# Kernel optimization log

Hardware: AMD Instinct MI355X
Metric: run time of the kernel (lower is better)

The kernel has to match this reference:

```python
import jax, jax.numpy as jnp
import numpy as np

DIM = 1024
HEADS = 16
HEAD_DIM = DIM // HEADS
SEQ = 2048
BATCH = 2


def setup_inputs() -> dict:
    key = jax.random.key(0)
    ks = jax.random.split(key, 9)
    s = 1.0 / np.sqrt(DIM)
    mk = lambda k: jax.random.uniform(k, (DIM, DIM), jnp.float32, -s, s)
    mb = lambda k: jax.random.uniform(k, (DIM,), jnp.float32, -s, s)
    return {
        "x": jax.random.normal(ks[0], (BATCH, SEQ, DIM), jnp.float32),
        "wq": mk(ks[1]), "bq": mb(ks[2]),
        "wk": mk(ks[3]), "bk": mb(ks[4]),
        "wv": mk(ks[5]), "bv": mb(ks[6]),
        "wo": mk(ks[7]), "bo": mb(ks[8]),
    }


def reference(x, wq, bq, wk, bk, wv, bv, wo, bo):
    b, s, d = x.shape
    inv_sqrt_hd = 1.0 / np.sqrt(HEAD_DIM)
    # torch Linear: y = x @ W.T + b
    q = (x @ wq.T + bq).reshape(b, s, HEADS, HEAD_DIM)
    k = (x @ wk.T + bk).reshape(b, s, HEADS, HEAD_DIM)
    v = (x @ wv.T + bv).reshape(b, s, HEADS, HEAD_DIM)
    # scores [b, h, s, s]; NOTE: original forward never applies the causal mask buffer
    scores = jnp.einsum("bqhd,bkhd->bhqk", q, k) * inv_sqrt_hd
    a = jax.nn.softmax(scores, axis=-1)
    o = jnp.einsum("bhqk,bkhd->bqhd", a, v).reshape(b, s, d)
    o = o @ wo.T + bo
    return (o, a.mean(axis=1))
```

## Files before the change

### kernel.cpp

```cpp
#include <hip/hip_runtime.h>
#include <stdint.h>

#define DIMD 1024
#define HEADS 16
#define HD 64
#define SEQ 2048
#define BATCH 2
#define MTOT (BATCH*SEQ)

typedef __attribute__((ext_vector_type(4))) float f32x4;
typedef __attribute__((ext_vector_type(8))) short bf16x8;
typedef __attribute__((ext_vector_type(8))) unsigned short ushort8;
typedef __attribute__((ext_vector_type(4))) unsigned short usx4;

#define GL_LDS16(gp, lp) __builtin_amdgcn_global_load_lds( \
    (const __attribute__((address_space(1))) unsigned int*)(gp), \
    (__attribute__((address_space(3))) unsigned int*)(lp), 16, 0, 0)

__device__ __forceinline__ unsigned short f2bf(float f) {
    unsigned int u = __builtin_bit_cast(unsigned int, f);
    u = (u + 0x7FFFu + ((u >> 16) & 1u)) >> 16;
    return (unsigned short)u;
}
__device__ __forceinline__ float bf2f(unsigned short s) {
    unsigned int u = ((unsigned int)s) << 16;
    return __builtin_bit_cast(float, u);
}

__global__ __launch_bounds__(256) void cvt_f32_bf16(const float* __restrict__ in,
                                                    unsigned short* __restrict__ out, int n) {
    int i = (blockIdx.x * 256 + threadIdx.x) * 8;
    if (i >= n) return;
    f32x4 a = *(const f32x4*)(in + i);
    f32x4 b = *(const f32x4*)(in + i + 4);
    ushort8 o;
    o[0] = f2bf(a[0]); o[1] = f2bf(a[1]); o[2] = f2bf(a[2]); o[3] = f2bf(a[3]);
    o[4] = f2bf(b[0]); o[5] = f2bf(b[1]); o[6] = f2bf(b[2]); o[7] = f2bf(b[3]);
    *(ushort8*)(out + i) = o;
}

__global__ __launch_bounds__(256) void cvt_w4(const float* __restrict__ w0, const float* __restrict__ w1,
                                              const float* __restrict__ w2, const float* __restrict__ w3,
                                              unsigned short* __restrict__ dst) {
    const int sel = blockIdx.x >> 9;
    const float* src = sel == 0 ? w0 : sel == 1 ? w1 : sel == 2 ? w2 : w3;
    int i = ((blockIdx.x & 511) * 256 + threadIdx.x) * 8;
    f32x4 a = *(const f32x4*)(src + i);
    f32x4 b = *(const f32x4*)(src + i + 4);
    ushort8 o;
    o[0] = f2bf(a[0]); o[1] = f2bf(a[1]); o[2] = f2bf(a[2]); o[3] = f2bf(a[3]);
    o[4] = f2bf(b[0]); o[5] = f2bf(b[1]); o[6] = f2bf(b[2]); o[7] = f2bf(b[3]);
    *(ushort8*)(dst + (size_t)sel * 1048576 + i) = o;
}

template<bool F32OUT>
__global__ __launch_bounds__(256, 2) void gemm_lds(const unsigned short* __restrict__ X,
                                                   const unsigned short* __restrict__ W,
                                                   const float* __restrict__ bias,
                                                   void* __restrict__ outp,
                                                   int Nv, int Kv) {
    __shared__ unsigned short As[2][128 * 64];
    __shared__ unsigned short Bs[2][64 * 64];
    const int tid = threadIdx.x, wid = tid >> 6;
    const int lane = tid & 63, lr = lane & 15, hi = lane >> 4;
    const int m0 = blockIdx.y * 128;
    const int n0 = blockIdx.x * 64;
    const int mq = (wid >> 1) * 64, nq = (wid & 1) * 32;
    const int NT = Kv >> 6;

    f32x4 acc[4][2];
    #pragma unroll
    for (int i = 0; i < 4; ++i)
        #pragma unroll
        for (int j = 0; j < 2; ++j) acc[i][j] = (f32x4){0.f, 0.f, 0.f, 0.f};

    #pragma unroll
    for (int it = 0; it < 4; ++it) {
        int li = it * 256 + tid, row = li >> 3, seg = li & 7;
        GL_LDS16(X + (size_t)(m0 + row) * Kv + ((seg ^ (row & 7)) << 3), &As[0][li * 8]);
    }
    #pragma unroll
    for (int it = 0; it < 2; ++it) {
        int li = it * 256 + tid, row = li >> 3, seg = li & 7;
        GL_LDS16(W + (size_t)(n0 + row) * Kv + ((seg ^ (row & 7)) << 3), &Bs[0][li * 8]);
    }
    __syncthreads();

    #pragma unroll 2
    for (int t = 0; t < NT; ++t) {
        const int cur = t & 1, nxt = cur ^ 1;
        if (t + 1 < NT) {
            const int k1 = (t + 1) << 6;
            #pragma unroll
            for (int it = 0; it < 4; ++it) {
                int li = it * 256 + tid, row = li >> 3, seg = li & 7;
                GL_LDS16(X + (size_t)(m0 + row) * Kv + k1 + ((seg ^ (row & 7)) << 3),
                         &As[nxt][li * 8]);
            }
            #pragma unroll
            for (int it = 0; it < 2; ++it) {
                int li = it * 256 + tid, row = li >> 3, seg = li & 7;
                GL_LDS16(W + (size_t)(n0 + row) * Kv + k1 + ((seg ^ (row & 7)) << 3),
                         &Bs[nxt][li * 8]);
            }
        }
        #pragma unroll
        for (int kk = 0; kk < 2; ++kk) {
            bf16x8 af[4], bfr[2];
            #pragma unroll
            for (int i = 0; i < 4; ++i) {
                int row = mq + 16 * i + lr;
                int seg = (kk * 4 + hi) ^ (row & 7);
                af[i] = *(const bf16x8*)(&As[cur][row * 64 + seg * 8]);
            }
            #pragma unroll
            for (int j = 0; j < 2; ++j) {
                int row = nq + 16 * j + lr;
                int seg = (kk * 4 + hi) ^ (row & 7);
                bfr[j] = *(const bf16x8*)(&Bs[cur][row * 64 + seg * 8]);
            }
            #pragma unroll
            for (int i = 0; i < 4; ++i)
                #pragma unroll
                for (int j = 0; j < 2; ++j)
                    acc[i][j] = __builtin_amdgcn_mfma_f32_16x16x32_bf16(af[i], bfr[j], acc[i][j], 0, 0, 0);
        }
        __syncthreads();
    }

    #pragma unroll
    for (int j = 0; j < 2; ++j) {
        const int col = n0 + nq + 16 * j + lr;
        const float bv = bias[col];
        #pragma unroll
        for (int i = 0; i < 4; ++i) {
            #pragma unroll
            for (int r = 0; r < 4; ++r) {
                const int row = m0 + mq + 16 * i + 4 * hi + r;
                float v = acc[i][j][r] + bv;
                if (F32OUT) ((float*)outp)[(size_t)row * Nv + col] = v;
                else        ((unsigned short*)outp)[(size_t)row * Nv + col] = f2bf(v);
            }
        }
    }
}

__global__ __launch_bounds__(256) void transpose_v(const unsigned short* __restrict__ v,
                                                   unsigned short* __restrict__ vT) {
    __shared__ unsigned short tile[64][72];
    const int bh = blockIdx.y;
    const int b = bh >> 4, h = bh & 15;
    const int s0 = blockIdx.x * 64;
    const int t = threadIdx.x;
    #pragma unroll
    for (int it = 0; it < 2; ++it) {
        int li = it * 256 + t;
        int row = li >> 3, c8 = (li & 7) * 8;
        ushort8 val = *(const ushort8*)(v + (size_t)(b * SEQ + s0 + row) * DIMD + h * HD + c8);
        *(ushort8*)&tile[row][c8] = val;
    }
    __syncthreads();
    #pragma unroll
    for (int it = 0; it < 2; ++it) {
        int li = it * 256 + t;
        int d = li >> 3, s8 = (li & 7) * 8;
        ushort8 o;
        #pragma unroll
        for (int j = 0; j < 8; ++j) o[j] = tile[s8 + j][d];
        *(ushort8*)(vT + (size_t)(bh * HD + d) * SEQ + s0 + s8) = o;
    }
}

__global__ __launch_bounds__(256, 4) void score_pv_kernel(const unsigned short* __restrict__ Q,
                                                          const unsigned short* __restrict__ Kt,
                                                          const unsigned short* __restrict__ vT,
                                                          unsigned short* __restrict__ Eb,
                                                          float* __restrict__ rlb,
                                                          unsigned short* __restrict__ attn, int b) {
    __shared__ unsigned short Ks[2][64 * 64];
    __shared__ unsigned short Vs[2][64 * 64];
    __shared__ unsigned short Es[32 * 68];
    __shared__ float ps[4][2][16];
    __shared__ float rls[32];
    const int tid = threadIdx.x, wid = tid >> 6, lane = tid & 63;
    const int lr = lane & 15, hi = lane >> 4;
    const int h = blockIdx.y;
    const int q0 = blockIdx.x * 32;
    const unsigned short* Kbase = Kt + (size_t)b * SEQ * DIMD + h * HD;
    const unsigned short* Vbase = vT + (size_t)(b * HEADS + h) * HD * SEQ;

    const unsigned short* qbase = Q + (size_t)(b * SEQ + q0) * DIMD + h * HD + 8 * hi;
    bf16x8 qb0[2], qb1[2];
    #pragma unroll
    for (int s = 0; s < 2; ++s) {
        const unsigned short* qp = qbase + (size_t)(16 * s + lr) * DIMD;
        qb0[s] = *(const bf16x8*)qp;
        qb1[s] = *(const bf16x8*)(qp + 32);
    }

    #pragma unroll
    for (int it = 0; it < 2; ++it) {
        int li = it * 256 + tid, row = li >> 3, seg = li & 7;
        GL_LDS16(Kbase + (size_t)row * DIMD + ((seg ^ (row & 7)) << 3), &Ks[0][li * 8]);
    }
    #pragma unroll
    for (int it = 0; it < 2; ++it) {
        int li = it * 256 + tid, row = li >> 3, seg = li & 7;
        GL_LDS16(Vbase + (size_t)row * SEQ + ((seg ^ (row & 7)) << 3), &Vs[0][li * 8]);
    }
    __syncthreads();

    float lsum[2] = {0.f, 0.f};
    f32x4 oacc[2];
    oacc[0] = (f32x4){0.f, 0.f, 0.f, 0.f};
    oacc[1] = (f32x4){0.f, 0.f, 0.f, 0.f};
    const int mq = (wid >> 1) * 16;
    const int nd = (wid & 1) * 32;
    const int erow = tid >> 3, ecol = (tid & 7) * 8;

    for (int t = 0; t < 32; ++t) {
        const int cur = t & 1, nxt = cur ^ 1;
        if (t + 1 < 32) {
            const int kb1 = (t + 1) * 64;
            #pragma unroll
            for (int it = 0; it < 2; ++it) {
                int li = it * 256 + tid, row = li >> 3, seg = li & 7;
                GL_LDS16(Kbase + (size_t)(kb1 + row) * DIMD + ((seg ^ (row & 7)) << 3),
                         &Ks[nxt][li * 8]);
            }
            #pragma unroll
            for (int it = 0; it < 2; ++it) {
                int li = it * 256 + tid, row = li >> 3, seg = li & 7;
                GL_LDS16(Vbase + (size_t)row * SEQ + kb1 + ((seg ^ (row & 7)) << 3),
                         &Vs[nxt][li * 8]);
            }
        }
        const int krow = wid * 16 + lr;
        bf16x8 a0 = *(const bf16x8*)(&Ks[cur][krow * 64 + ((hi       ^ (krow & 7)) << 3)]);
        bf16x8 a1 = *(const bf16x8*)(&Ks[cur][krow * 64 + (((4 + hi) ^ (krow & 7)) << 3)]);
        #pragma unroll
        for (int s = 0; s < 2; ++s) {
            f32x4 acc = (f32x4){0.f, 0.f, 0.f, 0.f};
            acc = __builtin_amdgcn_mfma_f32_16x16x32_bf16(a0, qb0[s], acc, 0, 0, 0);
            acc = __builtin_amdgcn_mfma_f32_16x16x32_bf16(a1, qb1[s], acc, 0, 0, 0);
            float e0 = __expf(acc[0] * 0.125f);
            float e1 = __expf(acc[1] * 0.125f);
            float e2 = __expf(acc[2] * 0.125f);
            float e3 = __expf(acc[3] * 0.125f);
            lsum[s] += (e0 + e1) + (e2 + e3);
            usx4 pk;
            pk[0] = f2bf(e0); pk[1] = f2bf(e1); pk[2] = f2bf(e2); pk[3] = f2bf(e3);
            *(usx4*)(&Es[(16 * s + lr) * 68 + wid * 16 + 4 * hi]) = pk;
        }
        __syncthreads();

        ushort8 ev = *(const ushort8*)(&Es[erow * 68 + ecol]);
        *(ushort8*)(Eb + ((size_t)h * SEQ + q0 + erow) * SEQ + t * 64 + ecol) = ev;

        #pragma unroll
        for (int kk = 0; kk < 2; ++kk) {
            bf16x8 ea = *(const bf16x8*)(&Es[(mq + lr) * 68 + kk * 32 + 8 * hi]);
            #pragma unroll
            for (int j = 0; j < 2; ++j) {
                int vrow = nd + 16 * j + lr;
                int seg = (kk * 4 + hi) ^ (vrow & 7);
                bf16x8 vb = *(const bf16x8*)(&Vs[cur][vrow * 64 + seg * 8]);
                oacc[j] = __builtin_amdgcn_mfma_f32_16x16x32_bf16(ea, vb, oacc[j], 0, 0, 0);
            }
        }
        __syncthreads();
    }

    #pragma unroll
    for (int s = 0; s < 2; ++s) {
        float l = lsum[s];
        l += __shfl_xor(l, 16);
        l += __shfl_xor(l, 32);
        if (lane < 16) ps[wid][s][lane] = l;
    }
    __syncthreads();
    if (tid < 32) {
        int s = tid >> 4, qq = tid & 15;
        float tot = ps[0][s][qq] + ps[1][s][qq] + ps[2][s][qq] + ps[3][s][qq];
        float r = 1.0f / tot;
        rlb[h * SEQ + q0 + 16 * s + qq] = r;
        rls[16 * s + qq] = r;
    }
    __syncthreads();

    #pragma unroll
    for (int r = 0; r < 4; ++r) {
        const int ql = mq + 4 * hi + r;
        const float rv = rls[ql];
        #pragma unroll
        for (int j = 0; j < 2; ++j)
            attn[(size_t)(b * SEQ + q0 + ql) * DIMD + h * HD + nd + 16 * j + lr] =
                f2bf(oacc[j][r] * rv);
    }
}

__global__ __launch_bounds__(256) void mean2_kernel(const unsigned short* __restrict__ Eb,
                                                    const float* __restrict__ rlb,
                                                    float* __restrict__ out1b) {
    __shared__ float rls[16];
    const int q = blockIdx.x, t = threadIdx.x;
    if (t < 16) rls[t] = rlb[t * SEQ + q] * 0.0625f;
    __syncthreads();
    const int k0 = t * 8;
    float acc[8] = {0.f, 0.f, 0.f, 0.f, 0.f, 0.f, 0.f, 0.f};
    #pragma unroll
    for (int h = 0; h < HEADS; ++h) {
        ushort8 e = *(const ushort8*)(Eb + ((size_t)h * SEQ + q) * SEQ + k0);
        float rv = rls[h];
        #pragma unroll
        for (int j = 0; j < 8; ++j) acc[j] += bf2f(e[j]) * rv;
    }
    f32x4 o0 = (f32x4){acc[0], acc[1], acc[2], acc[3]};
    f32x4 o1 = (f32x4){acc[4], acc[5], acc[6], acc[7]};
    *(f32x4*)(out1b + (size_t)q * SEQ + k0) = o0;
    *(f32x4*)(out1b + (size_t)q * SEQ + k0 + 4) = o1;
}

extern "C" void kernel_launch(void* const* d_in, const int* in_sizes, int n_in,
                              void* d_out, int out_size, void* d_ws, size_t ws_size,
                              hipStream_t stream) {
    const float* x  = (const float*)d_in[0];
    const float* wq = (const float*)d_in[1];
    const float* bq = (const float*)d_in[2];
    const float* wk = (const float*)d_in[3];
    const float* bk = (const float*)d_in[4];
    const float* wv = (const float*)d_in[5];
    const float* bv = (const float*)d_in[6];
    const float* wo = (const float*)d_in[7];
    const float* bo = (const float*)d_in[8];

    float* o_out    = (float*)d_out;
    float* mean_out = o_out + 4194304;

    unsigned short* xb   = (unsigned short*)d_ws;
    unsigned short* wqb  = xb   + 4194304;
    unsigned short* wkb  = wqb  + 1048576;
    unsigned short* wvb  = wkb  + 1048576;
    unsigned short* wob  = wvb  + 1048576;
    unsigned short* qb   = wob  + 1048576;
    unsigned short* kb   = qb   + 4194304;
    unsigned short* vTb  = kb   + 4194304;
    unsigned short* attb = vTb  + 4194304;
    float*          rlb  = (float*)(attb + 4194304);
    unsigned short* Eb   = (unsigned short*)(rlb + 65536);
    unsigned short* vb   = Eb;

    cvt_f32_bf16<<<2048, 256, 0, stream>>>(x, xb, 4194304);
    cvt_w4<<<2048, 256, 0, stream>>>(wq, wk, wv, wo, wqb);

    gemm_lds<false><<<dim3(16, 32), 256, 0, stream>>>(xb, wqb, bq, qb, DIMD, DIMD);
    gemm_lds<false><<<dim3(16, 32), 256, 0, stream>>>(xb, wkb, bk, kb, DIMD, DIMD);
    gemm_lds<false><<<dim3(16, 32), 256, 0, stream>>>(xb, wvb, bv, vb, DIMD, DIMD);
    transpose_v<<<dim3(32, 32), 256, 0, stream>>>(vb, vTb);

    for (int b = 0; b < BATCH; ++b) {
        float* rl_b = rlb + b * HEADS * SEQ;
        score_pv_kernel<<<dim3(64, 16), 256, 0, stream>>>(qb, kb, vTb, Eb, rl_b, attb, b);
        mean2_kernel<<<2048, 256, 0, stream>>>(Eb, rl_b, mean_out + (size_t)b * SEQ * SEQ);
    }

    gemm_lds<true><<<dim3(16, 32), 256, 0, stream>>>(attb, wob, bo, o_out, DIMD, DIMD);
}
```

Measured before the change: 224.3 us.

## Recompute QK scores for head-mean instead of storing exp matrix; fuse QKV GEMMs

Stops writing the per-head bf16 exp-score matrix (16x2048x2048 per batch) to global memory and re-reading it in the mean kernel. A new kernel recomputes QK^T per head with MFMA, exponentiates, scales by the stored reciprocal row sums, and accumulates the head mean in registers. It also merges the three Q/K/V projection GEMMs into one launch over a 48-wide grid. This trades a large memory round-trip for redundant score computation. It assumes the exp needs no max subtraction, which holds only if score_pv also uses raw exp.

```diff
diff --git a/kernel.cpp b/kernel.cpp
--- a/kernel.cpp
+++ b/kernel.cpp
@@ -54,6 +54,96 @@
 }
 
 template<bool F32OUT>
+__device__ __forceinline__ void gemm_body(const unsigned short* __restrict__ X,
+                                          const unsigned short* __restrict__ W,
+                                          const float* __restrict__ bias,
+                                          void* __restrict__ outp,
+                                          int m0, int n0, int Nv, int Kv,
+                                          unsigned short (*As)[128 * 64],
+                                          unsigned short (*Bs)[64 * 64]) {
+    const int tid = threadIdx.x, wid = tid >> 6;
+    const int lane = tid & 63, lr = lane & 15, hi = lane >> 4;
+    const int mq = (wid >> 1) * 64, nq = (wid & 1) * 32;
+    const int NT = Kv >> 6;
+
+    f32x4 acc[4][2];
+    #pragma unroll
+    for (int i = 0; i < 4; ++i)
+        #pragma unroll
+        for (int j = 0; j < 2; ++j) acc[i][j] = (f32x4){0.f, 0.f, 0.f, 0.f};
+
+    #pragma unroll
+    for (int it = 0; it < 4; ++it) {
+        int li = it * 256 + tid, row = li >> 3, seg = li & 7;
+        GL_LDS16(X + (size_t)(m0 + row) * Kv + ((seg ^ (row & 7)) << 3), &As[0][li * 8]);
+    }
+    #pragma unroll
+    for (int it = 0; it < 2; ++it) {
+        int li = it * 256 + tid, row = li >> 3, seg = li & 7;
+        GL_LDS16(W + (size_t)(n0 + row) * Kv + ((seg ^ (row & 7)) << 3), &Bs[0][li * 8]);
+    }
+    __syncthreads();
+
+    #pragma unroll 2
+    for (int t = 0; t < NT; ++t) {
+        const int cur = t & 1, nxt = cur ^ 1;
+        if (t + 1 < NT) {
+            const int k1 = (t + 1) << 6;
+            #pragma unroll
+            for (int it = 0; it < 4; ++it) {
+                int li = it * 256 + tid, row = li >> 3, seg = li & 7;
+                GL_LDS16(X + (size_t)(m0 + row) * Kv + k1 + ((seg ^ (row & 7)) << 3),
+                         &As[nxt][li * 8]);
+            }
+            #pragma unroll
+            for (int it = 0; it < 2; ++it) {
+                int li = it * 256 + tid, row = li >> 3, seg = li & 7;
+                GL_LDS16(W + (size_t)(n0 + row) * Kv + k1 + ((seg ^ (row & 7)) << 3),
+                         &Bs[nxt][li * 8]);
+            }
+        }
+        #pragma unroll
+        for (int kk = 0; kk < 2; ++kk) {
+            bf16x8 af[4], bfr[2];
+            #pragma unroll
+            for (int i = 0; i < 4; ++i) {
+                int row = mq + 16 * i + lr;
+                int seg = (kk * 4 + hi) ^ (row & 7);
+                af[i] = *(const bf16x8*)(&As[cur][row * 64 + seg * 8]);
+            }
+            #pragma unroll
+            for (int j = 0; j < 2; ++j) {
+                int row = nq + 16 * j + lr;
+                int seg = (kk * 4 + hi) ^ (row & 7);
+                bfr[j] = *(const bf16x8*)(&Bs[cur][row * 64 + seg * 8]);
+            }
+            #pragma unroll
+            for (int i = 0; i < 4; ++i)
+                #pragma unroll
+                for (int j = 0; j < 2; ++j)
+                    acc[i][j] = __builtin_amdgcn_mfma_f32_16x16x32_bf16(af[i], bfr[j], acc[i][j], 0, 0, 0);
+        }
+        __syncthreads();
+    }
+
+    #pragma unroll
+    for (int j = 0; j < 2; ++j) {
+        const int col = n0 + nq + 16 * j + lr;
+        const float bv = bias[col];
+        #pragma unroll
+        for (int i = 0; i < 4; ++i) {
+            #pragma unroll
+            for (int r = 0; r < 4; ++r) {
+                const int row = m0 + mq + 16 * i + 4 * hi + r;
+                float v = acc[i][j][r] + bv;
+                if (F32OUT) ((float*)outp)[(size_t)row * Nv + col] = v;
+                else        ((unsigned short*)outp)[(size_t)row * Nv + col] = f2bf(v);
+            }
+        }
+    }
+}
+
+template<bool F32OUT>
 __global__ __launch_bounds__(256, 2) void gemm_lds(const unsigned short* __restrict__ X,
                                                    const unsigned short* __restrict__ W,
                                                    const float* __restrict__ bias,
@@ -61,88 +151,25 @@
                                                    int Nv, int Kv) {
     __shared__ unsigned short As[2][128 * 64];
     __shared__ unsigned short Bs[2][64 * 64];
-    const int tid = threadIdx.x, wid = tid >> 6;
-    const int lane = tid & 63, lr = lane & 15, hi = lane >> 4;
-    const int m0 = blockIdx.y * 128;
-    const int n0 = blockIdx.x * 64;
-    const int mq = (wid >> 1) * 64, nq = (wid & 1) * 32;
-    const int NT = Kv >> 6;
-
-    f32x4 acc[4][2];
-    #pragma unroll
-    for (int i = 0; i < 4; ++i)
-        #pragma unroll
-        for (int j = 0; j < 2; ++j) acc[i][j] = (f32x4){0.f, 0.f, 0.f, 0.f};
-
-    #pragma unroll
-    for (int it = 0; it < 4; ++it) {
-        int li = it * 256 + tid, row = li >> 3, seg = li & 7;
-        GL_LDS16(X + (size_t)(m0 + row) * Kv + ((seg ^ (row & 7)) << 3), &As[0][li * 8]);
-    }
-    #pragma unroll
-    for (int it = 0; it < 2; ++it) {
-        int li = it * 256 + tid, row = li >> 3, seg = li & 7;
-        GL_LDS16(W + (size_t)(n0 + row) * Kv + ((seg ^ (row & 7)) << 3), &Bs[0][li * 8]);
-    }
-    __syncthreads();
-
-    #pragma unroll 2
-    for (int t = 0; t < NT; ++t) {
-        const int cur = t & 1, nxt = cur ^ 1;
-        if (t + 1 < NT) {
-            const int k1 = (t + 1) << 6;
-            #pragma unroll
-            for (int it = 0; it < 4; ++it) {
-                int li = it * 256 + tid, row = li >> 3, seg = li & 7;
-                GL_LDS16(X + (size_t)(m0 + row) * Kv + k1 + ((seg ^ (row & 7)) << 3),
-                         &As[nxt][li * 8]);
-            }
-            #pragma unroll
-            for (int it = 0; it < 2; ++it) {
-                int li = it * 256 + tid, row = li >> 3, seg = li & 7;
-                GL_LDS16(W + (size_t)(n0 + row) * Kv + k1 + ((seg ^ (row & 7)) << 3),
-                         &Bs[nxt][li * 8]);
-            }
-        }
-        #pragma unroll
-        for (int kk = 0; kk < 2; ++kk) {
-            bf16x8 af[4], bfr[2];
-            #pragma unroll
-            for (int i = 0; i < 4; ++i) {
-                int row = mq + 16 * i + lr;
-                int seg = (kk * 4 + hi) ^ (row & 7);
-                af[i] = *(const bf16x8*)(&As[cur][row * 64 + seg * 8]);
-            }
-            #pragma unroll
-            for (int j = 0; j < 2; ++j) {
-                int row = nq + 16 * j + lr;
-                int seg = (kk * 4 + hi) ^ (row & 7);
-                bfr[j] = *(const bf16x8*)(&Bs[cur][row * 64 + seg * 8]);
-            }
-            #pragma unroll
-            for (int i = 0; i < 4; ++i)
-                #pragma unroll
-                for (int j = 0; j < 2; ++j)
-                    acc[i][j] = __builtin_amdgcn_mfma_f32_16x16x32_bf16(af[i], bfr[j], acc[i][j], 0, 0, 0);
-        }
-        __syncthreads();
-    }
-
-    #pragma unroll
-    for (int j = 0; j < 2; ++j) {
-        const int col = n0 + nq + 16 * j + lr;
-        const float bv = bias[col];
-        #pragma unroll
-        for (int i = 0; i < 4; ++i) {
-            #pragma unroll
-            for (int r = 0; r < 4; ++r) {
-                const int row = m0 + mq + 16 * i + 4 * hi + r;
-                float v = acc[i][j][r] + bv;
-                if (F32OUT) ((float*)outp)[(size_t)row * Nv + col] = v;
-                else        ((unsigned short*)outp)[(size_t)row * Nv + col] = f2bf(v);
-            }
-        }
-    }
+    gemm_body<F32OUT>(X, W, bias, outp, blockIdx.y * 128, blockIdx.x * 64, Nv, Kv, As, Bs);
+}
+
+__global__ __launch_bounds__(256, 2) void gemm_qkv(const unsigned short* __restrict__ X,
+                                                   const unsigned short* __restrict__ Wall,
+                                                   const float* __restrict__ b0,
+                                                   const float* __restrict__ b1,
+                                                   const float* __restrict__ b2,
+                                                   unsigned short* __restrict__ o0,
+                                                   unsigned short* __restrict__ o1,
+                                                   unsigned short* __restrict__ o2) {
+    __shared__ unsigned short As[2][128 * 64];
+    __shared__ unsigned short Bs[2][64 * 64];
+    const int sel = blockIdx.x >> 4;
+    const int n0 = (blockIdx.x & 15) * 64;
+    const unsigned short* W = Wall + (size_t)sel * 1048576;
+    const float* bias = sel == 0 ? b0 : sel == 1 ? b1 : b2;
+    unsigned short* out = sel == 0 ? o0 : sel == 1 ? o1 : o2;
+    gemm_body<false>(X, W, bias, out, blockIdx.y * 128, n0, DIMD, DIMD, As, Bs);
 }
 
 __global__ __launch_bounds__(256) void transpose_v(const unsigned short* __restrict__ v,
@@ -174,7 +201,6 @@
 __global__ __launch_bounds__(256, 4) void score_pv_kernel(const unsigned short* __restrict__ Q,
                                                           const unsigned short* __restrict__ Kt,
                                                           const unsigned short* __restrict__ vT,
-                                                          unsigned short* __restrict__ Eb,
                                                           float* __restrict__ rlb,
                                                           unsigned short* __restrict__ attn, int b) {
     __shared__ unsigned short Ks[2][64 * 64];
@@ -216,7 +242,6 @@
     oacc[1] = (f32x4){0.f, 0.f, 0.f, 0.f};
     const int mq = (wid >> 1) * 16;
     const int nd = (wid & 1) * 32;
-    const int erow = tid >> 3, ecol = (tid & 7) * 8;
 
     for (int t = 0; t < 32; ++t) {
         const int cur = t & 1, nxt = cur ^ 1;
@@ -254,9 +279,6 @@
         }
         __syncthreads();
 
-        ushort8 ev = *(const ushort8*)(&Es[erow * 68 + ecol]);
-        *(ushort8*)(Eb + ((size_t)h * SEQ + q0 + erow) * SEQ + t * 64 + ecol) = ev;
-
         #pragma unroll
         for (int kk = 0; kk < 2; ++kk) {
             bf16x8 ea = *(const bf16x8*)(&Es[(mq + lr) * 68 + kk * 32 + 8 * hi]);
@@ -299,26 +321,77 @@
     }
 }
 
-__global__ __launch_bounds__(256) void mean2_kernel(const unsigned short* __restrict__ Eb,
-                                                    const float* __restrict__ rlb,
-                                                    float* __restrict__ out1b) {
-    __shared__ float rls[16];
-    const int q = blockIdx.x, t = threadIdx.x;
-    if (t < 16) rls[t] = rlb[t * SEQ + q] * 0.0625f;
-    __syncthreads();
-    const int k0 = t * 8;
-    float acc[8] = {0.f, 0.f, 0.f, 0.f, 0.f, 0.f, 0.f, 0.f};
-    #pragma unroll
+__global__ __launch_bounds__(256, 4) void mean_qk_kernel(const unsigned short* __restrict__ Q,
+                                                         const unsigned short* __restrict__ Kt,
+                                                         const float* __restrict__ rlb,
+                                                         float* __restrict__ out1b, int b) {
+    __shared__ unsigned short Ks[2][64 * 64];
+    const int tid = threadIdx.x, wid = tid >> 6, lane = tid & 63;
+    const int lr = lane & 15, hi = lane >> 4;
+    const int k0 = blockIdx.x * 256;
+    const int q0 = blockIdx.y * 32;
+    const unsigned short* Kb2 = Kt + (size_t)b * SEQ * DIMD;
+
+    f32x4 acc[4][2];
+    #pragma unroll
+    for (int c = 0; c < 4; ++c)
+        #pragma unroll
+        for (int g = 0; g < 2; ++g) acc[c][g] = (f32x4){0.f, 0.f, 0.f, 0.f};
+
+    #pragma unroll
+    for (int it = 0; it < 2; ++it) {
+        int li = it * 256 + tid, row = li >> 3, seg = li & 7;
+        GL_LDS16(Kb2 + (size_t)(k0 + row) * DIMD + ((seg ^ (row & 7)) << 3), &Ks[0][li * 8]);
+    }
+    __syncthreads();
+
     for (int h = 0; h < HEADS; ++h) {
-        ushort8 e = *(const ushort8*)(Eb + ((size_t)h * SEQ + q) * SEQ + k0);
-        float rv = rls[h];
-        #pragma unroll
-        for (int j = 0; j < 8; ++j) acc[j] += bf2f(e[j]) * rv;
-    }
-    f32x4 o0 = (f32x4){acc[0], acc[1], acc[2], acc[3]};
-    f32x4 o1 = (f32x4){acc[4], acc[5], acc[6], acc[7]};
-    *(f32x4*)(out1b + (size_t)q * SEQ + k0) = o0;
-    *(f32x4*)(out1b + (size_t)q * SEQ + k0 + 4) = o1;
+        const unsigned short* qbase = Q + (size_t)(b * SEQ + q0) * DIMD + h * HD + 8 * hi;
+        bf16x8 qb0[2], qb1[2];
+        float rlv[2];
+        #pragma unroll
+        for (int g = 0; g < 2; ++g) {
+            const unsigned short* qp = qbase + (size_t)(16 * g + lr) * DIMD;
+            qb0[g] = *(const bf16x8*)qp;
+            qb1[g] = *(const bf16x8*)(qp + 32);
+            rlv[g] = rlb[h * SEQ + q0 + 16 * g + lr] * 0.0625f;
+        }
+        #pragma unroll
+        for (int c = 0; c < 4; ++c) {
+            const int step = h * 4 + c;
+            const int cur = step & 1;
+            if (step + 1 < 64) {
+                const int s2 = step + 1, h2 = s2 >> 2, c2 = s2 & 3;
+                #pragma unroll
+                for (int it = 0; it < 2; ++it) {
+                    int li = it * 256 + tid, row = li >> 3, seg = li & 7;
+                    GL_LDS16(Kb2 + (size_t)(k0 + c2 * 64 + row) * DIMD + h2 * HD
+                                 + ((seg ^ (row & 7)) << 3),
+                             &Ks[s2 & 1][li * 8]);
+                }
+            }
+            const int krow = wid * 16 + lr;
+            bf16x8 a0 = *(const bf16x8*)(&Ks[cur][krow * 64 + ((hi       ^ (krow & 7)) << 3)]);
+            bf16x8 a1 = *(const bf16x8*)(&Ks[cur][krow * 64 + (((4 + hi) ^ (krow & 7)) << 3)]);
+            #pragma unroll
+            for (int g = 0; g < 2; ++g) {
+                f32x4 s = (f32x4){0.f, 0.f, 0.f, 0.f};
+                s = __builtin_amdgcn_mfma_f32_16x16x32_bf16(a0, qb0[g], s, 0, 0, 0);
+                s = __builtin_amdgcn_mfma_f32_16x16x32_bf16(a1, qb1[g], s, 0, 0, 0);
+                #pragma unroll
+                for (int r = 0; r < 4; ++r)
+                    acc[c][g][r] += __expf(s[r] * 0.125f) * rlv[g];
+            }
+            __syncthreads();
+        }
+    }
+
+    #pragma unroll
+    for (int c = 0; c < 4; ++c)
+        #pragma unroll
+        for (int g = 0; g < 2; ++g)
+            *(f32x4*)(out1b + (size_t)(q0 + 16 * g + lr) * SEQ
+                              + k0 + 64 * c + 16 * wid + 4 * hi) = acc[c][g];
 }
 
 extern "C" void kernel_launch(void* const* d_in, const int* in_sizes, int n_in,
@@ -347,21 +420,19 @@
     unsigned short* vTb  = kb   + 4194304;
     unsigned short* attb = vTb  + 4194304;
     float*          rlb  = (float*)(attb + 4194304);
-    unsigned short* Eb   = (unsigned short*)(rlb + 65536);
-    unsigned short* vb   = Eb;
+    unsigned short* vb   = (unsigned short*)(rlb + 65536);
 
     cvt_f32_bf16<<<2048, 256, 0, stream>>>(x, xb, 4194304);
     cvt_w4<<<2048, 256, 0, stream>>>(wq, wk, wv, wo, wqb);
 
-    gemm_lds<false><<<dim3(16, 32), 256, 0, stream>>>(xb, wqb, bq, qb, DIMD, DIMD);
-    gemm_lds<false><<<dim3(16, 32), 256, 0, stream>>>(xb, wkb, bk, kb, DIMD, DIMD);
-    gemm_lds<false><<<dim3(16, 32), 256, 0, stream>>>(xb, wvb, bv, vb, DIMD, DIMD);
+    gemm_qkv<<<dim3(48, 32), 256, 0, stream>>>(xb, wqb, bq, bk, bv, qb, kb, vb);
     transpose_v<<<dim3(32, 32), 256, 0, stream>>>(vb, vTb);
 
     for (int b = 0; b < BATCH; ++b) {
         float* rl_b = rlb + b * HEADS * SEQ;
-        score_pv_kernel<<<dim3(64, 16), 256, 0, stream>>>(qb, kb, vTb, Eb, rl_b, attb, b);
-        mean2_kernel<<<2048, 256, 0, stream>>>(Eb, rl_b, mean_out + (size_t)b * SEQ * SEQ);
+        score_pv_kernel<<<dim3(64, 16), 256, 0, stream>>>(qb, kb, vTb, rl_b, attb, b);
+        mean_qk_kernel<<<dim3(8, 64), 256, 0, stream>>>(qb, kb, rl_b,
+                                                        mean_out + (size_t)b * SEQ * SEQ, b);
     }
 
     gemm_lds<true><<<dim3(16, 32), 256, 0, stream>>>(attb, wob, bo, o_out, DIMD, DIMD);
```

Measured after the change: 243.3 us. 8.5% more time.
